# Performance work log

Measured on AMD Instinct MI355X. Metric: run time of the kernel, lower is better.

The kernel has to match this reference:

```python
import jax, jax.numpy as jnp
import numpy as np

NUM_HEADS = 16
HEAD_DIM = 64
BATCH = 4
SEQ = 1024
MAX_SEQ_LEN = 2048


def _shift(pos_score):
    # Transformer-XL relative shift. pos_score: (NH, S, S_kv)
    NH, S, S_kv = pos_score.shape
    zero_pad = jnp.zeros((NH, S, 1), dtype=pos_score.dtype)
    padded = jnp.concatenate([zero_pad, pos_score], axis=-1)  # (NH, S, S_kv+1)
    padded = padded.reshape(NH, S_kv + 1, S)
    return padded[:, 1:, :].reshape(NH, S, S_kv)


def setup_inputs() -> dict:
    key = jax.random.key(0)
    ks = jax.random.split(key, 6)
    NH = BATCH * NUM_HEADS
    return {
        "queries": jax.random.normal(ks[0], (NH, SEQ, HEAD_DIM), dtype=jnp.float32),
        "keys": jax.random.normal(ks[1], (NH, SEQ, HEAD_DIM), dtype=jnp.float32),
        "values": jax.random.normal(ks[2], (NH, SEQ, HEAD_DIM), dtype=jnp.float32),
        "u_bias": jax.random.normal(ks[3], (1, NUM_HEADS, 1, HEAD_DIM), dtype=jnp.float32),
        "v_bias": jax.random.normal(ks[4], (1, NUM_HEADS, 1, HEAD_DIM), dtype=jnp.float32),
        "R": jax.random.normal(ks[5], (NUM_HEADS, MAX_SEQ_LEN, HEAD_DIM), dtype=jnp.float32),
    }


def reference(queries, keys, values, u_bias, v_bias, R):
    NH, S, d = queries.shape
    S_kv = keys.shape[1]
    batch = NH // NUM_HEADS

    q = queries * (d ** -0.5)
    q = q.reshape(batch, NUM_HEADS, S, d)
    q_u = (q + u_bias).reshape(NH, S, d)
    q_v = (q + v_bias).reshape(NH, S, d)

    # relative position embeddings, tiled over batch: (NH, S_kv, d)
    R_s = jnp.tile(R[:, :S_kv, :], (batch, 1, 1))

    content_score = jnp.einsum('nsd,ntd->nst', q_u, keys)   # (NH, S, S_kv)
    pos_score = jnp.einsum('nsd,ntd->nst', q_v, R_s)        # (NH, S, S_kv)
    pos_score = _shift(pos_score)

    attn_weights = jax.nn.softmax(content_score + pos_score, axis=-1)
    attn = jnp.einsum('nst,ntd->nsd', attn_weights, values)  # (NH, S, d)
    return attn
```

## Files before the change

kernel.cpp:

```cpp
#include <hip/hip_runtime.h>


#define SQ    1024
#define HD    64
#define NHD   16
#define RMAX  2048

typedef _Float16 f16x8 __attribute__((ext_vector_type(8)));
typedef _Float16 f16x4 __attribute__((ext_vector_type(4)));
typedef short    b16x8 __attribute__((ext_vector_type(8)));
typedef float    f32x4 __attribute__((ext_vector_type(4)));

#define MFMA_F16(A,B,C)  __builtin_amdgcn_mfma_f32_16x16x32_f16((A),(B),(C),0,0,0)
#define MFMA_BF16(A,B,C) __builtin_amdgcn_mfma_f32_16x16x32_bf16((A),(B),(C),0,0,0)

#define L2E 1.44269504088896f

#define KH_OFF   0
#define VT_OFF   (8u << 20)
#define R16_OFF  (18u << 20)
#define WS_NEED  (20u << 20)

__device__ __forceinline__ float exp2fast(float x) {
#if __has_builtin(__builtin_amdgcn_exp2f)
  return __builtin_amdgcn_exp2f(x);
#else
  return __expf(x * 0.693147180559945f);
#endif
}

__device__ __forceinline__ short f2b(float f) {
  unsigned u = __builtin_bit_cast(unsigned, f);
  u += 0x7FFFu + ((u >> 16) & 1u);
  return (short)(u >> 16);
}
__device__ __forceinline__ unsigned pkh(float a, float b) {
  _Float16 h0 = (_Float16)a, h1 = (_Float16)b;
  return (unsigned)__builtin_bit_cast(unsigned short, h0)
       | ((unsigned)__builtin_bit_cast(unsigned short, h1) << 16);
}
__device__ __forceinline__ unsigned pkb2(float a, float b) {
  unsigned ua = __builtin_bit_cast(unsigned, a) + 0x8000u;
  unsigned ub = __builtin_bit_cast(unsigned, b) + 0x8000u;
  return (ub & 0xFFFF0000u) | (ua >> 16);
}


__global__ __launch_bounds__(256) void preprep(
    const float* __restrict__ K, const float* __restrict__ R,
    const float* __restrict__ V,
    _Float16* __restrict__ Kh, _Float16* __restrict__ R16,
    short* __restrict__ Vt)
{
  __shared__ float t[64][65];
  const int bid = blockIdx.x, tid = threadIdx.x;
  if (bid < 1024) {
    const int n = bid >> 4, st = bid & 15;
    {
      const int row = tid >> 2, c0 = (tid & 3) * 16;
      const float* src = V + ((size_t)n * SQ + st * 64 + row) * HD + c0;
#pragma unroll
      for (int i = 0; i < 4; ++i) {
        float4 x = ((const float4*)src)[i];
        t[row][c0 + 4*i + 0] = x.x; t[row][c0 + 4*i + 1] = x.y;
        t[row][c0 + 4*i + 2] = x.z; t[row][c0 + 4*i + 3] = x.w;
      }
    }
    __syncthreads();
    {
      const int d = tid >> 2, s0 = (tid & 3) * 16;
      short* dst = Vt + ((size_t)n * 80 + d) * SQ + st * 64 + s0;
#pragma unroll
      for (int i = 0; i < 8; ++i)
        *(unsigned*)(dst + 2*i) = pkb2(t[s0 + 2*i][d], t[s0 + 2*i + 1][d]);
    }
    if (tid < 64) {
      const int s = st * 64 + tid;
      Vt[((size_t)n * 80 + 64) * SQ + s] = (short)0x3F80;
#pragma unroll
      for (int r = 65; r < 80; ++r) Vt[((size_t)n * 80 + r) * SQ + s] = 0;
    }
  } else {
    const int idx = (bid - 1024) * 256 + tid;
    const int nk4 = (64 * SQ * HD) / 4;
    if (idx < nk4) {
      float4 v = ((const float4*)K)[idx];
      f16x4 o = { (_Float16)v.x, (_Float16)v.y, (_Float16)v.z, (_Float16)v.w };
      *(f16x4*)(Kh + 4 * (size_t)idx) = o;
    } else {
      int rr = idx - nk4;
      int h  = rr >> 14, off = rr & 16383;
      float4 v = ((const float4*)R)[((size_t)h << 15) + off];
      f16x4 o = { (_Float16)v.x, (_Float16)v.y, (_Float16)v.z, (_Float16)v.w };
      *(f16x4*)(R16 + 4 * (((size_t)h << 14) + off)) = o;
    }
  }
}


__global__ __launch_bounds__(256, 4) void relpos_sdpa_r9(
    const float* __restrict__ Q, const _Float16* __restrict__ Kh,
    const short* __restrict__ Vtg, const _Float16* __restrict__ R16,
    const float* __restrict__ Ub, const float* __restrict__ Vb,
    float* __restrict__ O)
{
  const int n    = blockIdx.x;
  const int h    = n & (NHD - 1);
  const int a0   = blockIdx.y * 64;
  const int tid  = threadIdx.x;
  const int lane = tid & 63, wave = tid >> 6;
  const int l15  = lane & 15, quad = lane >> 4;

  const float*    Qn  = Q   + (size_t)n * SQ * HD;
  const _Float16* Khn = Kh  + (size_t)n * SQ * HD;
  const short*    Vgn = Vtg + (size_t)n * 80 * SQ;
  const _Float16* Rh  = R16 + (size_t)h * SQ * HD;

  __shared__ __align__(16) char lds[47128];
  _Float16*       Kb  = (_Float16*)lds;
  short*          Vt  = (short*)(lds + 9216);
  unsigned short* Ps  = (unsigned short*)(lds + 9216 + 11520);
  unsigned*       Pb2 = (unsigned*)(lds + 9216 + 11520 + 8704);
  const _Float16* Pb2h = (const _Float16*)Pb2;

  f16x8 quF[2], qvF[5][2];
#pragma unroll
  for (int ks = 0; ks < 2; ++ks) {
    const int db = ks * 32 + quad * 8;
    float ub[8], vb[8];
#pragma unroll
    for (int j = 0; j < 8; ++j) {
      ub[j] = Ub[h*HD + db + j] * L2E;
      vb[j] = Vb[h*HD + db + j] * L2E;
    }
    {
      const float* p = Qn + (size_t)(a0 + 16*wave + l15) * HD + db;
      float4 x0 = ((const float4*)p)[0], x1 = ((const float4*)p)[1];
      f16x8 f;
#pragma unroll
      for (int t = 0; t < 4; ++t) {
        f[t]   = (_Float16)((&x0.x)[t] * (0.125f * L2E) + ub[t]);
        f[t+4] = (_Float16)((&x1.x)[t] * (0.125f * L2E) + ub[t+4]);
      }
      quF[ks] = f;
    }
#pragma unroll
    for (int rt = 0; rt < 5; ++rt) {
      int row = a0 + 16*rt + l15; if (row > SQ-1) row = SQ-1;
      const float* p = Qn + (size_t)row * HD + db;
      float4 x0 = ((const float4*)p)[0], x1 = ((const float4*)p)[1];
      f16x8 f;
#pragma unroll
      for (int t = 0; t < 4; ++t) {
        f[t]   = (_Float16)((&x0.x)[t] * (0.125f * L2E) + vb[t]);
        f[t+4] = (_Float16)((&x1.x)[t] * (0.125f * L2E) + vb[t+4]);
      }
      qvF[rt][ks] = f;
    }
  }

  if (tid < 64) Vt[64*72 + tid] = (short)0x3F80;

  f32x4 Oacc[5];
#pragma unroll
  for (int ct = 0; ct < 5; ++ct) Oacc[ct] = (f32x4){0.f, 0.f, 0.f, 0.f};

  unsigned ringW[9];
  int ringSlot;
  auto band = [&](int jstart) {
    const int c    = jstart + 16*wave + l15;
    const int j    = (c + 2048) & (SQ - 1);
    ringSlot       = (c + 2048) & 127;
    const _Float16* rp = Rh + (size_t)j * HD + quad * 8;
    f16x8 B0 = *(const f16x8*)rp;
    f16x8 B1 = *(const f16x8*)(rp + 32);
#pragma unroll
    for (int rt = 0; rt < 5; ++rt) {
      f32x4 acc = (f32x4){0.f, 0.f, 0.f, 0.f};
      acc = MFMA_F16(qvF[rt][0], B0, acc);
      acc = MFMA_F16(qvF[rt][1], B1, acc);
      if (rt < 4) {
        ringW[2*rt]     = pkh(acc[0], acc[1]);
        ringW[2*rt + 1] = pkh(acc[2], acc[3]);
      } else {
        ringW[8] = pkh(acc[0], acc[1]);
      }
    }
  };
  auto ringFlush = [&]() {
#pragma unroll
    for (int rt = 0; rt < 4; ++rt) {
      const int rp0 = 8*rt + 2*quad;
      Pb2[rp0*134 + ringSlot]       = ringW[2*rt];
      Pb2[(rp0 + 1)*134 + ringSlot] = ringW[2*rt + 1];
    }
    if (quad == 0) Pb2[32*134 + ringSlot] = ringW[8];
  };

  band(-a0 - 65);  ringFlush();
  band(-a0 - 1);   ringFlush();

  f16x8 kPre[2]; b16x8 vPre[2];
  auto stageLoad = [&](int k0) {
    const _Float16* ks = Khn + (size_t)(k0 + lane) * HD + wave*8;
    kPre[0] = *(const f16x8*)ks;
    kPre[1] = *(const f16x8*)(ks + 32);
    const short* vs = Vgn + (size_t)lane * SQ + k0 + wave*8;
    vPre[0] = *(const b16x8*)vs;
    vPre[1] = *(const b16x8*)(vs + 32);
  };
  auto stageWrite = [&]() {
    *(f16x8*)&Kb[lane*72 + wave*8]      = kPre[0];
    *(f16x8*)&Kb[lane*72 + wave*8 + 32] = kPre[1];
    *(b16x8*)&Vt[lane*72 + wave*8]      = vPre[0];
    *(b16x8*)&Vt[lane*72 + wave*8 + 32] = vPre[1];
  };

  stageLoad(0);

  const int iiB = 16*wave + 4*quad;

  for (int k0 = 0; k0 < SQ; k0 += 64) {
    __syncthreads();

    stageWrite();
    if (k0 > 0) ringFlush();

    __syncthreads();

    if (k0 < SQ - 64) stageLoad(k0 + 64);

    f32x4 sc[4];
#pragma unroll
    for (int ct = 0; ct < 4; ++ct) {
      f16x8 b0 = *(const f16x8*)&Kb[(16*ct + l15)*72 + quad*8];
      f16x8 b1 = *(const f16x8*)&Kb[(16*ct + l15)*72 + 32 + quad*8];
      f32x4 acc = (f32x4){0.f, 0.f, 0.f, 0.f};
      acc = MFMA_F16(quF[0], b0, acc);
      acc = MFMA_F16(quF[1], b1, acc);
      sc[ct] = acc;
    }

    const int dlt = k0 - a0;
#pragma unroll
    for (int r = 0; r < 4; ++r) {
      const int ii = iiB + r;
      const int adA = (ii >> 1) * 268 + (ii & 1);
      const int adB = ((ii + 1) >> 1) * 268 + ((ii + 1) & 1);
#pragma unroll
      for (int ct = 0; ct < 4; ++ct) {
        const int e    = dlt + 16*ct + l15 - ii;
        const int u    = (e > 0) ? 1 : 0;
        const int slot = (e - 1 - u) & 127;
        float pos = (float)Pb2h[(u ? adB : adA) + 2*slot];
        float s   = sc[ct][r] + ((e == 1) ? 0.f : pos);
        sc[ct][r] = exp2fast(s - 57.7078016f);
      }
    }

#pragma unroll
    for (int r = 0; r < 4; ++r) {
      unsigned w0 = pkb2(sc[0][r], sc[1][r]);
      unsigned w1 = pkb2(sc[2][r], sc[3][r]);
      const int pbase = (iiB + r)*68 + l15;
      Ps[pbase]      = (unsigned short)w0;
      Ps[pbase + 16] = (unsigned short)(w0 >> 16);
      Ps[pbase + 32] = (unsigned short)w1;
      Ps[pbase + 48] = (unsigned short)(w1 >> 16);
    }

    b16x8 pA0 = *(const b16x8*)&Ps[(16*wave + l15)*68 + quad*8];
    b16x8 pA1 = *(const b16x8*)&Ps[(16*wave + l15)*68 + 32 + quad*8];
#pragma unroll
    for (int ct = 0; ct < 5; ++ct) {
      b16x8 v0 = *(const b16x8*)&Vt[(16*ct + l15)*72 + quad*8];
      b16x8 v1 = *(const b16x8*)&Vt[(16*ct + l15)*72 + 32 + quad*8];
      Oacc[ct] = MFMA_BF16(pA0, v0, Oacc[ct]);
      Oacc[ct] = MFMA_BF16(pA1, v1, Oacc[ct]);
    }

    if (k0 < SQ - 64) band(k0 + 64 - a0 - 1);
  }

#pragma unroll
  for (int r = 0; r < 4; ++r) {
    float l   = __shfl(Oacc[4][r], lane & 48);
    float inv = 1.0f / l;
    const size_t rowo = (size_t)n * SQ * HD + (size_t)(a0 + iiB + r) * HD;
#pragma unroll
    for (int ct = 0; ct < 4; ++ct)
      O[rowo + 16*ct + l15] = Oacc[ct][r] * inv;
  }
}


__global__ __launch_bounds__(256, 4) void relpos_sdpa_fb(
    const float* __restrict__ Q, const float* __restrict__ K,
    const float* __restrict__ V, const float* __restrict__ Ub,
    const float* __restrict__ Vb, const float* __restrict__ R,
    float* __restrict__ O)
{
  const int n    = blockIdx.x;
  const int h    = n & (NHD - 1);
  const int a0   = blockIdx.y * 64;
  const int tid  = threadIdx.x;
  const int lane = tid & 63, wave = tid >> 6;
  const int l15  = lane & 15, quad = lane >> 4;

  const float* Qn = Q + (size_t)n * SQ * HD;
  const float* Kn = K + (size_t)n * SQ * HD;
  const float* Vn = V + (size_t)n * SQ * HD;
  const float* Rh = R + (size_t)h * RMAX * HD;

  __shared__ __align__(16) char lds[38656];
  _Float16* Kb = (_Float16*)lds;
  short*    Ps = (short*)lds;
  short*    Vt = (short*)(lds + 9216);
  _Float16* Pb = (_Float16*)(lds + 9216 + 11520);

  f16x8 quF[2], qvF[5][2];
#pragma unroll
  for (int ks = 0; ks < 2; ++ks) {
    const int db = ks * 32 + quad * 8;
    float ub[8], vb[8];
#pragma unroll
    for (int j = 0; j < 8; ++j) { ub[j] = Ub[h*HD + db + j]; vb[j] = Vb[h*HD + db + j]; }
    {
      const float* p = Qn + (size_t)(a0 + 16*wave + l15) * HD + db;
      f16x8 f;
#pragma unroll
      for (int j = 0; j < 8; ++j) f[j] = (_Float16)(p[j] * 0.125f + ub[j]);
      quF[ks] = f;
    }
#pragma unroll
    for (int rt = 0; rt < 5; ++rt) {
      int row = a0 + 16*rt + l15; if (row > SQ-1) row = SQ-1;
      const float* p = Qn + (size_t)row * HD + db;
      f16x8 f;
#pragma unroll
      for (int j = 0; j < 8; ++j) f[j] = (_Float16)(p[j] * 0.125f + vb[j]);
      qvF[rt][ks] = f;
    }
  }

  if (tid < 64) Vt[64*72 + tid] = (short)0x3F80;

  f32x4 Oacc[5];
#pragma unroll
  for (int ct = 0; ct < 5; ++ct) Oacc[ct] = (f32x4){0.f, 0.f, 0.f, 0.f};

  auto band = [&](int jstart) {
    const int c    = jstart + 16*wave + l15;
    const int j    = (c + 2048) & (SQ - 1);
    const int slot = (c + 2048) & 127;
    const float* rp = Rh + (size_t)j * HD + quad * 8;
    f16x8 B0, B1;
    {
      float4 x0 = *(const float4*)(rp),      x1 = *(const float4*)(rp + 4);
      float4 y0 = *(const float4*)(rp + 32), y1 = *(const float4*)(rp + 36);
#pragma unroll
      for (int t = 0; t < 4; ++t) { B0[t] = (_Float16)(&x0.x)[t]; B0[t+4] = (_Float16)(&x1.x)[t]; }
#pragma unroll
      for (int t = 0; t < 4; ++t) { B1[t] = (_Float16)(&y0.x)[t]; B1[t+4] = (_Float16)(&y1.x)[t]; }
    }
#pragma unroll
    for (int rt = 0; rt < 5; ++rt) {
      f32x4 acc = (f32x4){0.f, 0.f, 0.f, 0.f};
      acc = MFMA_F16(qvF[rt][0], B0, acc);
      acc = MFMA_F16(qvF[rt][1], B1, acc);
      const int row = 16*rt + 4*quad;
      if (rt < 4) {
        *(unsigned*)&Pb[slot*70 + row]     = pkh(acc[0], acc[1]);
        *(unsigned*)&Pb[slot*70 + row + 2] = pkh(acc[2], acc[3]);
      } else if (quad == 0) {
        *(unsigned*)&Pb[slot*70 + row]     = pkh(acc[0], acc[1]);
      }
    }
  };

  band(-a0 - 65);
  band(-a0 - 1);

  const int sr = tid >> 2, sc4 = tid & 3;
  const int iiB = 16*wave + 4*quad;

  for (int k0 = 0; k0 < SQ; k0 += 64) {
    __syncthreads();
    {
      const float* src = Kn + (size_t)(k0 + sr) * HD + sc4 * 16;
      float4 x0 = *(const float4*)(src),     x1 = *(const float4*)(src + 4);
      float4 y0 = *(const float4*)(src + 8), y1 = *(const float4*)(src + 12);
      f16x8 lo, hi;
#pragma unroll
      for (int t = 0; t < 4; ++t) { lo[t] = (_Float16)(&x0.x)[t]; lo[t+4] = (_Float16)(&x1.x)[t]; }
#pragma unroll
      for (int t = 0; t < 4; ++t) { hi[t] = (_Float16)(&y0.x)[t]; hi[t+4] = (_Float16)(&y1.x)[t]; }
      *(f16x8*)&Kb[sr*72 + sc4*16]     = lo;
      *(f16x8*)&Kb[sr*72 + sc4*16 + 8] = hi;
    }
    {
      const int g = lane >> 3;
#pragma unroll
      for (int i = 0; i < 8; ++i) {
        int bp = 8*wave + (i ^ g);
        float v0 = Vn[(size_t)(k0 + 2*bp)     * HD + lane];
        float v1 = Vn[(size_t)(k0 + 2*bp + 1) * HD + lane];
        *(unsigned*)&Vt[lane*72 + 2*bp] = pkb2(v0, v1);
      }
    }
    __syncthreads();

    f32x4 sc[4];
#pragma unroll
    for (int ct = 0; ct < 4; ++ct) {
      f16x8 b0 = *(const f16x8*)&Kb[(16*ct + l15)*72 + quad*8];
      f16x8 b1 = *(const f16x8*)&Kb[(16*ct + l15)*72 + 32 + quad*8];
      f32x4 acc = (f32x4){0.f, 0.f, 0.f, 0.f};
      acc = MFMA_F16(quF[0], b0, acc);
      acc = MFMA_F16(quF[1], b1, acc);
      sc[ct] = acc;
    }

    const int dlt = k0 - a0;
#pragma unroll
    for (int r = 0; r < 4; ++r) {
      const int ii = iiB + r;
#pragma unroll
      for (int ct = 0; ct < 4; ++ct) {
        const int e    = dlt + 16*ct + l15 - ii;
        const int u    = (e > 0) ? 1 : 0;
        const int slot = (e - 1 - u + 2048) & 127;
        float pos = (float)Pb[slot*70 + ii + u];
        float s   = sc[ct][r] + ((e == 1) ? 0.f : pos);
        sc[ct][r] = __expf(s - 40.0f);
      }
    }
    __syncthreads();

#pragma unroll
    for (int r = 0; r < 4; ++r)
#pragma unroll
      for (int ct = 0; ct < 4; ++ct)
        Ps[(iiB + r)*68 + 16*ct + l15] = f2b(sc[ct][r]);

    b16x8 pA0 = *(const b16x8*)&Ps[(16*wave + l15)*68 + quad*8];
    b16x8 pA1 = *(const b16x8*)&Ps[(16*wave + l15)*68 + 32 + quad*8];
#pragma unroll
    for (int ct = 0; ct < 5; ++ct) {
      b16x8 v0 = *(const b16x8*)&Vt[(16*ct + l15)*72 + quad*8];
      b16x8 v1 = *(const b16x8*)&Vt[(16*ct + l15)*72 + 32 + quad*8];
      Oacc[ct] = MFMA_BF16(pA0, v0, Oacc[ct]);
      Oacc[ct] = MFMA_BF16(pA1, v1, Oacc[ct]);
    }

    if (k0 < SQ - 64) band(k0 + 64 - a0 - 1);
  }

#pragma unroll
  for (int r = 0; r < 4; ++r) {
    float l   = __shfl(Oacc[4][r], lane & 48);
    float inv = 1.0f / l;
    const size_t rowo = (size_t)n * SQ * HD + (size_t)(a0 + iiB + r) * HD;
#pragma unroll
    for (int ct = 0; ct < 4; ++ct)
      O[rowo + 16*ct + l15] = Oacc[ct][r] * inv;
  }
}

extern "C" void kernel_launch(void* const* d_in, const int* in_sizes, int n_in,
                              void* d_out, int out_size, void* d_ws, size_t ws_size,
                              hipStream_t stream) {
  const float* Q  = (const float*)d_in[0];
  const float* K  = (const float*)d_in[1];
  const float* V  = (const float*)d_in[2];
  const float* Ub = (const float*)d_in[3];
  const float* Vb = (const float*)d_in[4];
  const float* R  = (const float*)d_in[5];
  float* O = (float*)d_out;

  if (ws_size >= WS_NEED) {
    _Float16* Kh  = (_Float16*)((char*)d_ws + KH_OFF);
    short*    Vt  = (short*)((char*)d_ws + VT_OFF);
    _Float16* R16 = (_Float16*)((char*)d_ws + R16_OFF);

    preprep<<<6144, 256, 0, stream>>>(K, R, V, Kh, R16, Vt);

    dim3 grid(64, 16);
    relpos_sdpa_r9<<<grid, 256, 0, stream>>>(Q, Kh, Vt, R16, Ub, Vb, O);
  } else {
    dim3 grid(64, 16);
    relpos_sdpa_fb<<<grid, 256, 0, stream>>>(Q, K, V, Ub, Vb, R, O);
  }
}
```

Measured before the change: 196.9 us.

## Load K and V MFMA operands directly from global instead of LDS staging

Removes the register-prefetched LDS staging of K and transposed V tiles. Each wave now reads its MFMA B operands straight from the preconverted global buffers. This eliminates the LDS writes and reads for K/V and shrinks the shared-memory footprint, which could allow more resident blocks. In exchange, all four waves fetch the same K/V data redundantly through the cache, and the loads are no longer prefetched one iteration ahead, so their latency is exposed right before the MFMAs.

```diff
diff --git a/kernel.cpp b/kernel.cpp
--- a/kernel.cpp
+++ b/kernel.cpp
@@ -98,7 +98,7 @@
 }
 
 
-__global__ __launch_bounds__(256, 4) void relpos_sdpa_r9(
+__global__ __launch_bounds__(256, 4) void relpos_sdpa_r10(
     const float* __restrict__ Q, const _Float16* __restrict__ Kh,
     const short* __restrict__ Vtg, const _Float16* __restrict__ R16,
     const float* __restrict__ Ub, const float* __restrict__ Vb,
@@ -116,11 +116,9 @@
   const short*    Vgn = Vtg + (size_t)n * 80 * SQ;
   const _Float16* Rh  = R16 + (size_t)h * SQ * HD;
 
-  __shared__ __align__(16) char lds[47128];
-  _Float16*       Kb  = (_Float16*)lds;
-  short*          Vt  = (short*)(lds + 9216);
-  unsigned short* Ps  = (unsigned short*)(lds + 9216 + 11520);
-  unsigned*       Pb2 = (unsigned*)(lds + 9216 + 11520 + 8704);
+  __shared__ __align__(16) char lds[26392];
+  unsigned short* Ps   = (unsigned short*)lds;
+  unsigned*       Pb2  = (unsigned*)(lds + 8704);
   const _Float16* Pb2h = (const _Float16*)Pb2;
 
   f16x8 quF[2], qvF[5][2];
@@ -158,8 +156,6 @@
       qvF[rt][ks] = f;
     }
   }
-
-  if (tid < 64) Vt[64*72 + tid] = (short)0x3F80;
 
   f32x4 Oacc[5];
 #pragma unroll
@@ -200,41 +196,21 @@
   band(-a0 - 65);  ringFlush();
   band(-a0 - 1);   ringFlush();
 
-  f16x8 kPre[2]; b16x8 vPre[2];
-  auto stageLoad = [&](int k0) {
-    const _Float16* ks = Khn + (size_t)(k0 + lane) * HD + wave*8;
-    kPre[0] = *(const f16x8*)ks;
-    kPre[1] = *(const f16x8*)(ks + 32);
-    const short* vs = Vgn + (size_t)lane * SQ + k0 + wave*8;
-    vPre[0] = *(const b16x8*)vs;
-    vPre[1] = *(const b16x8*)(vs + 32);
-  };
-  auto stageWrite = [&]() {
-    *(f16x8*)&Kb[lane*72 + wave*8]      = kPre[0];
-    *(f16x8*)&Kb[lane*72 + wave*8 + 32] = kPre[1];
-    *(b16x8*)&Vt[lane*72 + wave*8]      = vPre[0];
-    *(b16x8*)&Vt[lane*72 + wave*8 + 32] = vPre[1];
-  };
-
-  stageLoad(0);
-
   const int iiB = 16*wave + 4*quad;
 
   for (int k0 = 0; k0 < SQ; k0 += 64) {
     __syncthreads();
 
-    stageWrite();
     if (k0 > 0) ringFlush();
 
     __syncthreads();
 
-    if (k0 < SQ - 64) stageLoad(k0 + 64);
-
     f32x4 sc[4];
 #pragma unroll
     for (int ct = 0; ct < 4; ++ct) {
-      f16x8 b0 = *(const f16x8*)&Kb[(16*ct + l15)*72 + quad*8];
-      f16x8 b1 = *(const f16x8*)&Kb[(16*ct + l15)*72 + 32 + quad*8];
+      const _Float16* kp = Khn + (size_t)(k0 + 16*ct + l15) * HD + quad*8;
+      f16x8 b0 = *(const f16x8*)kp;
+      f16x8 b1 = *(const f16x8*)(kp + 32);
       f32x4 acc = (f32x4){0.f, 0.f, 0.f, 0.f};
       acc = MFMA_F16(quF[0], b0, acc);
       acc = MFMA_F16(quF[1], b1, acc);
@@ -271,10 +247,12 @@
 
     b16x8 pA0 = *(const b16x8*)&Ps[(16*wave + l15)*68 + quad*8];
     b16x8 pA1 = *(const b16x8*)&Ps[(16*wave + l15)*68 + 32 + quad*8];
+
 #pragma unroll
     for (int ct = 0; ct < 5; ++ct) {
-      b16x8 v0 = *(const b16x8*)&Vt[(16*ct + l15)*72 + quad*8];
-      b16x8 v1 = *(const b16x8*)&Vt[(16*ct + l15)*72 + 32 + quad*8];
+      const short* vp = Vgn + (size_t)(16*ct + l15) * SQ + k0 + quad*8;
+      b16x8 v0 = *(const b16x8*)vp;
+      b16x8 v1 = *(const b16x8*)(vp + 32);
       Oacc[ct] = MFMA_BF16(pA0, v0, Oacc[ct]);
       Oacc[ct] = MFMA_BF16(pA1, v1, Oacc[ct]);
     }
@@ -486,7 +464,7 @@
     preprep<<<6144, 256, 0, stream>>>(K, R, V, Kh, R16, Vt);
 
     dim3 grid(64, 16);
-    relpos_sdpa_r9<<<grid, 256, 0, stream>>>(Q, Kh, Vt, R16, Ub, Vb, O);
+    relpos_sdpa_r10<<<grid, 256, 0, stream>>>(Q, Kh, Vt, R16, Ub, Vb, O);
   } else {
     dim3 grid(64, 16);
     relpos_sdpa_fb<<<grid, 256, 0, stream>>>(Q, K, V, Ub, Vb, R, O);
```

Measured after the change: 256.7 us. +30.3%, slower.

## Swizzle LDS tiles, fold softmax shift into MFMA init, specialize off-diagonal position lookup

Applied to the files above, without the earlier changes.

Replaces padded LDS row strides for the K, V^T and P tiles with an XOR-swizzled unpadded layout, which shrinks shared memory and avoids bank conflicts. It also tightens the ring-buffer stride. The constant softmax shift is now the MFMA accumulator's initial value instead of a per-element subtraction. Away from the two diagonal-crossing tiles, the relative-position gather uses a simpler branch-free address computation without the e==1 special case. The risk is that the swizzle indexing adds integer ALU work, and the tile-dependent branch adds a little code size.

```diff
diff --git a/kernel.cpp b/kernel.cpp
--- a/kernel.cpp
+++ b/kernel.cpp
@@ -14,7 +14,8 @@
 #define MFMA_F16(A,B,C)  __builtin_amdgcn_mfma_f32_16x16x32_f16((A),(B),(C),0,0,0)
 #define MFMA_BF16(A,B,C) __builtin_amdgcn_mfma_f32_16x16x32_bf16((A),(B),(C),0,0,0)
 
-#define L2E 1.44269504088896f
+#define L2E    1.44269504088896f
+#define NSHIFT (-57.7078016f)
 
 #define KH_OFF   0
 #define VT_OFF   (8u << 20)
@@ -43,6 +44,9 @@
   unsigned ua = __builtin_bit_cast(unsigned, a) + 0x8000u;
   unsigned ub = __builtin_bit_cast(unsigned, b) + 0x8000u;
   return (ub & 0xFFFF0000u) | (ua >> 16);
+}
+__device__ __forceinline__ int swz(int row, int col) {
+  return row*64 + ((((col >> 3) ^ row) & 7) << 3) + (col & 7);
 }
 
 
@@ -98,7 +102,7 @@
 }
 
 
-__global__ __launch_bounds__(256, 4) void relpos_sdpa_r9(
+__global__ __launch_bounds__(256, 4) void relpos_sdpa_r11(
     const float* __restrict__ Q, const _Float16* __restrict__ Kh,
     const short* __restrict__ Vtg, const _Float16* __restrict__ R16,
     const float* __restrict__ Ub, const float* __restrict__ Vb,
@@ -116,11 +120,11 @@
   const short*    Vgn = Vtg + (size_t)n * 80 * SQ;
   const _Float16* Rh  = R16 + (size_t)h * SQ * HD;
 
-  __shared__ __align__(16) char lds[47128];
-  _Float16*       Kb  = (_Float16*)lds;
-  short*          Vt  = (short*)(lds + 9216);
-  unsigned short* Ps  = (unsigned short*)(lds + 9216 + 11520);
-  unsigned*       Pb2 = (unsigned*)(lds + 9216 + 11520 + 8704);
+  __shared__ __align__(16) char lds[42128];
+  _Float16*       Kb   = (_Float16*)lds;
+  short*          Vt   = (short*)(lds + 8192);
+  unsigned short* Ps   = (unsigned short*)(lds + 16512);
+  unsigned*       Pb2  = (unsigned*)(lds + 24704);
   const _Float16* Pb2h = (const _Float16*)Pb2;
 
   f16x8 quF[2], qvF[5][2];
@@ -159,7 +163,7 @@
     }
   }
 
-  if (tid < 64) Vt[64*72 + tid] = (short)0x3F80;
+  if (tid < 64) Vt[swz(64, tid)] = (short)0x3F80;
 
   f32x4 Oacc[5];
 #pragma unroll
@@ -191,10 +195,10 @@
 #pragma unroll
     for (int rt = 0; rt < 4; ++rt) {
       const int rp0 = 8*rt + 2*quad;
-      Pb2[rp0*134 + ringSlot]       = ringW[2*rt];
-      Pb2[(rp0 + 1)*134 + ringSlot] = ringW[2*rt + 1];
-    }
-    if (quad == 0) Pb2[32*134 + ringSlot] = ringW[8];
+      Pb2[rp0*132 + ringSlot]       = ringW[2*rt];
+      Pb2[(rp0 + 1)*132 + ringSlot] = ringW[2*rt + 1];
+    }
+    if (quad == 0) Pb2[32*132 + ringSlot] = ringW[8];
   };
 
   band(-a0 - 65);  ringFlush();
@@ -210,10 +214,10 @@
     vPre[1] = *(const b16x8*)(vs + 32);
   };
   auto stageWrite = [&]() {
-    *(f16x8*)&Kb[lane*72 + wave*8]      = kPre[0];
-    *(f16x8*)&Kb[lane*72 + wave*8 + 32] = kPre[1];
-    *(b16x8*)&Vt[lane*72 + wave*8]      = vPre[0];
-    *(b16x8*)&Vt[lane*72 + wave*8 + 32] = vPre[1];
+    *(f16x8*)&Kb[swz(lane, wave*8)]      = kPre[0];
+    *(f16x8*)&Kb[swz(lane, 32 + wave*8)] = kPre[1];
+    *(b16x8*)&Vt[swz(lane, wave*8)]      = vPre[0];
+    *(b16x8*)&Vt[swz(lane, 32 + wave*8)] = vPre[1];
   };
 
   stageLoad(0);
@@ -233,28 +237,45 @@
     f32x4 sc[4];
 #pragma unroll
     for (int ct = 0; ct < 4; ++ct) {
-      f16x8 b0 = *(const f16x8*)&Kb[(16*ct + l15)*72 + quad*8];
-      f16x8 b1 = *(const f16x8*)&Kb[(16*ct + l15)*72 + 32 + quad*8];
-      f32x4 acc = (f32x4){0.f, 0.f, 0.f, 0.f};
+      f16x8 b0 = *(const f16x8*)&Kb[swz(16*ct + l15, quad*8)];
+      f16x8 b1 = *(const f16x8*)&Kb[swz(16*ct + l15, 32 + quad*8)];
+      f32x4 acc = (f32x4){NSHIFT, NSHIFT, NSHIFT, NSHIFT};
       acc = MFMA_F16(quF[0], b0, acc);
       acc = MFMA_F16(quF[1], b1, acc);
       sc[ct] = acc;
     }
 
     const int dlt = k0 - a0;
-#pragma unroll
-    for (int r = 0; r < 4; ++r) {
-      const int ii = iiB + r;
-      const int adA = (ii >> 1) * 268 + (ii & 1);
-      const int adB = ((ii + 1) >> 1) * 268 + ((ii + 1) & 1);
-#pragma unroll
-      for (int ct = 0; ct < 4; ++ct) {
-        const int e    = dlt + 16*ct + l15 - ii;
-        const int u    = (e > 0) ? 1 : 0;
-        const int slot = (e - 1 - u) & 127;
-        float pos = (float)Pb2h[(u ? adB : adA) + 2*slot];
-        float s   = sc[ct][r] + ((e == 1) ? 0.f : pos);
-        sc[ct][r] = exp2fast(s - 57.7078016f);
+    if (dlt == 0 || dlt == 64) {
+#pragma unroll
+      for (int r = 0; r < 4; ++r) {
+        const int ii = iiB + r;
+        const int adA = (ii >> 1) * 264 + (ii & 1);
+        const int adB = ((ii + 1) >> 1) * 264 + ((ii + 1) & 1);
+#pragma unroll
+        for (int ct = 0; ct < 4; ++ct) {
+          const int e    = dlt + 16*ct + l15 - ii;
+          const int u    = (e > 0) ? 1 : 0;
+          const int slot = (e - 1 - u) & 127;
+          float pos = (float)Pb2h[(u ? adB : adA) + 2*slot];
+          float s   = sc[ct][r] + ((e == 1) ? 0.f : pos);
+          sc[ct][r] = exp2fast(s);
+        }
+      }
+    } else {
+      const int uu    = (dlt > 0) ? 1 : 0;
+      const int cbase = dlt - 1 - uu + l15 - iiB + 2048;
+#pragma unroll
+      for (int r = 0; r < 4; ++r) {
+        const int iu = iiB + r + uu;
+        const int ad = (iu >> 1) * 264 + (iu & 1);
+        const int c0 = cbase - r;
+#pragma unroll
+        for (int ct = 0; ct < 4; ++ct) {
+          const int slot = (c0 + 16*ct) & 127;
+          float pos = (float)Pb2h[ad + 2*slot];
+          sc[ct][r] = exp2fast(sc[ct][r] + pos);
+        }
       }
     }
 
@@ -262,19 +283,19 @@
     for (int r = 0; r < 4; ++r) {
       unsigned w0 = pkb2(sc[0][r], sc[1][r]);
       unsigned w1 = pkb2(sc[2][r], sc[3][r]);
-      const int pbase = (iiB + r)*68 + l15;
-      Ps[pbase]      = (unsigned short)w0;
-      Ps[pbase + 16] = (unsigned short)(w0 >> 16);
-      Ps[pbase + 32] = (unsigned short)w1;
-      Ps[pbase + 48] = (unsigned short)(w1 >> 16);
-    }
-
-    b16x8 pA0 = *(const b16x8*)&Ps[(16*wave + l15)*68 + quad*8];
-    b16x8 pA1 = *(const b16x8*)&Ps[(16*wave + l15)*68 + 32 + quad*8];
+      const int row = iiB + r;
+      Ps[swz(row, l15)]      = (unsigned short)w0;
+      Ps[swz(row, 16 + l15)] = (unsigned short)(w0 >> 16);
+      Ps[swz(row, 32 + l15)] = (unsigned short)w1;
+      Ps[swz(row, 48 + l15)] = (unsigned short)(w1 >> 16);
+    }
+
+    b16x8 pA0 = *(const b16x8*)&Ps[swz(16*wave + l15, quad*8)];
+    b16x8 pA1 = *(const b16x8*)&Ps[swz(16*wave + l15, 32 + quad*8)];
 #pragma unroll
     for (int ct = 0; ct < 5; ++ct) {
-      b16x8 v0 = *(const b16x8*)&Vt[(16*ct + l15)*72 + quad*8];
-      b16x8 v1 = *(const b16x8*)&Vt[(16*ct + l15)*72 + 32 + quad*8];
+      b16x8 v0 = *(const b16x8*)&Vt[swz(16*ct + l15, quad*8)];
+      b16x8 v1 = *(const b16x8*)&Vt[swz(16*ct + l15, 32 + quad*8)];
       Oacc[ct] = MFMA_BF16(pA0, v0, Oacc[ct]);
       Oacc[ct] = MFMA_BF16(pA1, v1, Oacc[ct]);
     }
@@ -486,7 +507,7 @@
     preprep<<<6144, 256, 0, stream>>>(K, R, V, Kh, R16, Vt);
 
     dim3 grid(64, 16);
-    relpos_sdpa_r9<<<grid, 256, 0, stream>>>(Q, Kh, Vt, R16, Ub, Vb, O);
+    relpos_sdpa_r11<<<grid, 256, 0, stream>>>(Q, Kh, Vt, R16, Ub, Vb, O);
   } else {
     dim3 grid(64, 16);
     relpos_sdpa_fb<<<grid, 256, 0, stream>>>(Q, K, V, Ub, Vb, R, O);
```

Result: faster. 177.7 us (-9.7%).
